# Kernel tuning notes

Hardware: AMD Instinct MI355X
Metric: run time of the kernel (lower is better)

Reference implementation:

```python
import jax, jax.numpy as jnp
import numpy as np

B = 1024
U = 2048

def setup_inputs() -> dict:
    key = jax.random.key(0)
    k1, k2, k3, k4 = jax.random.split(key, 4)
    x = jax.random.normal(k1, (B, U), dtype=jnp.float32)
    h = jax.random.normal(k2, (B, U), dtype=jnp.float32)
    c = jax.random.normal(k3, (B, U), dtype=jnp.float32)
    # keras 'uniform' initializer ~ U(-0.05, 0.05); scale similarly
    w = jax.random.uniform(k4, (2 * U, 4 * U), dtype=jnp.float32, minval=-0.05, maxval=0.05)
    return {"x": x, "h": h, "c": c, "w": w}

def reference(x, h, c, w):
    # concat -> matmul -> split into 4 gates -> gating
    xh = jnp.concatenate([x, h], axis=1)            # [B, 2U]
    ifgo = xh @ w                                   # [B, 4U]
    i, f, g, o = jnp.split(ifgo, 4, axis=1)
    i = jax.nn.sigmoid(i)
    f = jax.nn.sigmoid(f)
    o = jax.nn.sigmoid(o)
    g = jnp.tanh(g)
    c_new = f * c + i * g
    h_new = o * jnp.tanh(c_new)
    return (h_new, h_new, c_new)
```

## Files before the change

kernel.cpp:

```cpp
#include <hip/hip_runtime.h>


#define BDIM   1024
#define UDIM   2048
#define KDIM   4096
#define NDIM   8192

#define BM 128
#define BN 128
#define BK 64
#define NT (KDIM / BK)

typedef __attribute__((ext_vector_type(4))) float        f32x4;
typedef __attribute__((ext_vector_type(8))) short        short8;
typedef __attribute__((ext_vector_type(4))) unsigned int u32x4;

__device__ inline unsigned int cvt_pk_bf16(float lo, float hi) {
    unsigned int r;
    asm("v_cvt_pk_bf16_f32 %0, %1, %2" : "=v"(r) : "v"(lo), "v"(hi));
    return r;
}

__global__ __launch_bounds__(256, 2)
void lstm_gemm(const float* __restrict__ x, const float* __restrict__ h,
               const float* __restrict__ w, float* __restrict__ ifgo) {
    __shared__ unsigned short As[2][BM * BK];
    __shared__ unsigned short Bs[2][BN * BK];

    const int tid  = threadIdx.x;
    const int lane = tid & 63;
    const int wid  = tid >> 6;
    const int wr   = wid >> 1;
    const int wc   = wid & 1;
    const int lrow = lane & 15;
    const int lk   = lane >> 4;

    const int m0 = blockIdx.y * BM;
    const int n0 = blockIdx.x * BN;

    f32x4 acc[4][4];
#pragma unroll
    for (int i = 0; i < 4; ++i)
#pragma unroll
        for (int j = 0; j < 4; ++j)
            acc[i][j] = (f32x4){0.f, 0.f, 0.f, 0.f};

    f32x4 av[4][2];
    float bv[4][8];

    auto loadA = [&](int t) {
        int k0 = t * BK;
        const float* src = (k0 < UDIM) ? x + (size_t)m0 * UDIM + k0
                                       : h + (size_t)m0 * UDIM + (k0 - UDIM);
#pragma unroll
        for (int p = 0; p < 4; ++p) {
            int e = p * 256 + tid, arow = e >> 3, k8 = (e & 7) * 8;
            const float* gp = src + (size_t)arow * UDIM + k8;
            av[p][0] = *(const f32x4*)gp;
            av[p][1] = *(const f32x4*)(gp + 4);
        }
    };
    auto loadB = [&](int t) {
        int k0 = t * BK;
#pragma unroll
        for (int p = 0; p < 4; ++p) {
            int q = p * 256 + tid, n = q & 127, kg = q >> 7;
            const float* gp = w + (size_t)(k0 + kg * 8) * NDIM + n0 + n;
#pragma unroll
            for (int j = 0; j < 8; ++j) bv[p][j] = gp[(size_t)j * NDIM];
        }
    };
    auto writeAB = [&](int buf) {
        char* AsB = (char*)As[buf];
        char* BsB = (char*)Bs[buf];
#pragma unroll
        for (int p = 0; p < 4; ++p) {
            int e = p * 256 + tid, arow = e >> 3, k8 = (e & 7) * 8;
            u32x4 u;
            u[0] = cvt_pk_bf16(av[p][0][0], av[p][0][1]);
            u[1] = cvt_pk_bf16(av[p][0][2], av[p][0][3]);
            u[2] = cvt_pk_bf16(av[p][1][0], av[p][1][1]);
            u[3] = cvt_pk_bf16(av[p][1][2], av[p][1][3]);
            *(u32x4*)(AsB + arow * 128 + ((k8 * 2) ^ ((arow & 7) << 4))) = u;
        }
#pragma unroll
        for (int p = 0; p < 4; ++p) {
            int q = p * 256 + tid, n = q & 127, kg = q >> 7;
            u32x4 u;
#pragma unroll
            for (int j = 0; j < 4; ++j)
                u[j] = cvt_pk_bf16(bv[p][2 * j], bv[p][2 * j + 1]);
            *(u32x4*)(BsB + n * 128 + ((kg * 16) ^ ((n & 7) << 4))) = u;
        }
    };
    auto compute = [&](int buf) {
        const char* AsB = (const char*)As[buf];
        const char* BsB = (const char*)Bs[buf];
#pragma unroll
        for (int kk = 0; kk < 2; ++kk) {
            short8 af[4], bfr[4];
#pragma unroll
            for (int mi = 0; mi < 4; ++mi) {
                int row = wr * 64 + mi * 16 + lrow;
                int kb  = kk * 64 + lk * 16;
                af[mi] = *(const short8*)(AsB + row * 128 + (kb ^ ((row & 7) << 4)));
            }
#pragma unroll
            for (int ni = 0; ni < 4; ++ni) {
                int row = wc * 64 + ni * 16 + lrow;
                int kb  = kk * 64 + lk * 16;
                bfr[ni] = *(const short8*)(BsB + row * 128 + (kb ^ ((row & 7) << 4)));
            }
#pragma unroll
            for (int mi = 0; mi < 4; ++mi)
#pragma unroll
                for (int ni = 0; ni < 4; ++ni)
                    acc[mi][ni] = __builtin_amdgcn_mfma_f32_16x16x32_bf16(
                        af[mi], bfr[ni], acc[mi][ni], 0, 0, 0);
        }
    };

    loadA(0); loadB(0);
    writeAB(0);
    loadA(1); loadB(1);
    __syncthreads();

    for (int t = 0; t < NT; ++t) {
        int cur = t & 1;
        if (t + 1 < NT) {
            writeAB(cur ^ 1);
            if (t + 2 < NT) { loadA(t + 2); loadB(t + 2); }
        }
        compute(cur);
        __syncthreads();
    }

#pragma unroll
    for (int mi = 0; mi < 4; ++mi) {
        int grow = m0 + wr * 64 + mi * 16 + lk * 4;
#pragma unroll
        for (int ni = 0; ni < 4; ++ni) {
            int gcol = n0 + wc * 64 + ni * 16 + lrow;
            float* op = ifgo + (size_t)grow * NDIM + gcol;
#pragma unroll
            for (int r = 0; r < 4; ++r)
                op[(size_t)r * NDIM] = acc[mi][ni][r];
        }
    }
}

__device__ inline float fast_sigmoid(float v) {
    return __builtin_amdgcn_rcpf(1.f + __expf(-v));
}
__device__ inline float fast_tanh(float v) {
    float t = __expf(-2.f * __builtin_fabsf(v));
    float r = (1.f - t) * __builtin_amdgcn_rcpf(1.f + t);
    return __builtin_copysignf(r, v);
}

__global__ __launch_bounds__(256)
void lstm_gates(const float* __restrict__ ifgo, const float* __restrict__ c,
                float* __restrict__ out) {
    const int total4 = (BDIM * UDIM) / 4;
    int idx = blockIdx.x * blockDim.x + threadIdx.x;
    if (idx >= total4) return;
    int m  = idx >> 9;
    int u4 = idx & 511;
    const f32x4* base = (const f32x4*)(ifgo + (size_t)m * NDIM);
    f32x4 iv = base[u4];
    f32x4 fv = base[512 + u4];
    f32x4 gv = base[1024 + u4];
    f32x4 ov = base[1536 + u4];
    f32x4 cv = ((const f32x4*)c)[idx];
    f32x4 hn, cn;
#pragma unroll
    for (int r = 0; r < 4; ++r) {
        float ii = fast_sigmoid(iv[r]);
        float ff = fast_sigmoid(fv[r]);
        float oo = fast_sigmoid(ov[r]);
        float gg = fast_tanh(gv[r]);
        float cc = ff * cv[r] + ii * gg;
        cn[r] = cc;
        hn[r] = oo * fast_tanh(cc);
    }
    ((f32x4*)out)[idx] = hn;
    ((f32x4*)(out + (size_t)BDIM * UDIM))[idx] = hn;
    ((f32x4*)(out + (size_t)2 * BDIM * UDIM))[idx] = cn;
}

extern "C" void kernel_launch(void* const* d_in, const int* in_sizes, int n_in,
                              void* d_out, int out_size, void* d_ws, size_t ws_size,
                              hipStream_t stream) {
    const float* x = (const float*)d_in[0];
    const float* h = (const float*)d_in[1];
    const float* c = (const float*)d_in[2];
    const float* w = (const float*)d_in[3];
    float* ifgo = (float*)d_ws;
    float* out  = (float*)d_out;

    dim3 ggrid(NDIM / BN, BDIM / BM);
    lstm_gemm<<<ggrid, 256, 0, stream>>>(x, h, w, ifgo);

    int total4 = (BDIM * UDIM) / 4;
    lstm_gates<<<(total4 + 255) / 256, 256, 0, stream>>>(ifgo, c, out);
}
```

Measured before the change: 294.4 us.

## Fuse LSTM gate activations into GEMM epilogue by gathering all four gates per tile

Each GEMM tile now takes 32 units from each of the four gate column ranges, so one block holds i, f, g and o for the same units and applies the LSTM gating in its epilogue. This removes the 32 MB ifgo intermediate write and read and the second kernel launch. The warp layout changes from 2x2 to 4x1 (each warp covers 32 rows by 128 columns), which means more B fragment LDS reads per MFMA. The epilogue stores are now scalar and strided rather than vectorised.

```diff
diff --git a/kernel.cpp b/kernel.cpp
--- a/kernel.cpp
+++ b/kernel.cpp
@@ -5,9 +5,7 @@
 #define UDIM   2048
 #define KDIM   4096
 #define NDIM   8192
-
 #define BM 128
-#define BN 128
 #define BK 64
 #define NT (KDIM / BK)
 
@@ -20,29 +18,36 @@
     asm("v_cvt_pk_bf16_f32 %0, %1, %2" : "=v"(r) : "v"(lo), "v"(hi));
     return r;
 }
+__device__ inline float fast_sigmoid(float v) {
+    return __builtin_amdgcn_rcpf(1.f + __expf(-v));
+}
+__device__ inline float fast_tanh(float v) {
+    float t = __expf(-2.f * __builtin_fabsf(v));
+    float r = (1.f - t) * __builtin_amdgcn_rcpf(1.f + t);
+    return __builtin_copysignf(r, v);
+}
 
 __global__ __launch_bounds__(256, 2)
-void lstm_gemm(const float* __restrict__ x, const float* __restrict__ h,
-               const float* __restrict__ w, float* __restrict__ ifgo) {
+void lstm_fused(const float* __restrict__ x, const float* __restrict__ h,
+                const float* __restrict__ c, const float* __restrict__ w,
+                float* __restrict__ out) {
     __shared__ unsigned short As[2][BM * BK];
-    __shared__ unsigned short Bs[2][BN * BK];
+    __shared__ unsigned short Bs[2][BM * BK];
 
     const int tid  = threadIdx.x;
     const int lane = tid & 63;
     const int wid  = tid >> 6;
-    const int wr   = wid >> 1;
-    const int wc   = wid & 1;
     const int lrow = lane & 15;
     const int lk   = lane >> 4;
 
     const int m0 = blockIdx.y * BM;
-    const int n0 = blockIdx.x * BN;
+    const int u0 = blockIdx.x * 32;
 
-    f32x4 acc[4][4];
+    f32x4 acc[2][8];
 #pragma unroll
-    for (int i = 0; i < 4; ++i)
+    for (int i = 0; i < 2; ++i)
 #pragma unroll
-        for (int j = 0; j < 4; ++j)
+        for (int j = 0; j < 8; ++j)
             acc[i][j] = (f32x4){0.f, 0.f, 0.f, 0.f};
 
     f32x4 av[4][2];
@@ -64,8 +69,9 @@
         int k0 = t * BK;
 #pragma unroll
         for (int p = 0; p < 4; ++p) {
-            int q = p * 256 + tid, n = q & 127, kg = q >> 7;
-            const float* gp = w + (size_t)(k0 + kg * 8) * NDIM + n0 + n;
+            int q = p * 256 + tid, np = q & 127, kg = q >> 7;
+            int col = (np >> 5) * UDIM + u0 + (np & 31);
+            const float* gp = w + (size_t)(k0 + kg * 8) * NDIM + col;
 #pragma unroll
             for (int j = 0; j < 8; ++j) bv[p][j] = gp[(size_t)j * NDIM];
         }
@@ -85,12 +91,12 @@
         }
 #pragma unroll
         for (int p = 0; p < 4; ++p) {
-            int q = p * 256 + tid, n = q & 127, kg = q >> 7;
+            int q = p * 256 + tid, np = q & 127, kg = q >> 7;
             u32x4 u;
 #pragma unroll
             for (int j = 0; j < 4; ++j)
                 u[j] = cvt_pk_bf16(bv[p][2 * j], bv[p][2 * j + 1]);
-            *(u32x4*)(BsB + n * 128 + ((kg * 16) ^ ((n & 7) << 4))) = u;
+            *(u32x4*)(BsB + np * 128 + ((kg * 16) ^ ((np & 7) << 4))) = u;
         }
     };
     auto compute = [&](int buf) {
@@ -98,23 +104,22 @@
         const char* BsB = (const char*)Bs[buf];
 #pragma unroll
         for (int kk = 0; kk < 2; ++kk) {
-            short8 af[4], bfr[4];
+            short8 af[2], bfr[8];
+            int kb = kk * 64 + lk * 16;
 #pragma unroll
-            for (int mi = 0; mi < 4; ++mi) {
-                int row = wr * 64 + mi * 16 + lrow;
-                int kb  = kk * 64 + lk * 16;
+            for (int mi = 0; mi < 2; ++mi) {
+                int row = wid * 32 + mi * 16 + lrow;
                 af[mi] = *(const short8*)(AsB + row * 128 + (kb ^ ((row & 7) << 4)));
             }
 #pragma unroll
-            for (int ni = 0; ni < 4; ++ni) {
-                int row = wc * 64 + ni * 16 + lrow;
-                int kb  = kk * 64 + lk * 16;
+            for (int ni = 0; ni < 8; ++ni) {
+                int row = ni * 16 + lrow;
                 bfr[ni] = *(const short8*)(BsB + row * 128 + (kb ^ ((row & 7) << 4)));
             }
 #pragma unroll
-            for (int mi = 0; mi < 4; ++mi)
+            for (int mi = 0; mi < 2; ++mi)
 #pragma unroll
-                for (int ni = 0; ni < 4; ++ni)
+                for (int ni = 0; ni < 8; ++ni)
                     acc[mi][ni] = __builtin_amdgcn_mfma_f32_16x16x32_bf16(
                         af[mi], bfr[ni], acc[mi][ni], 0, 0, 0);
         }
@@ -135,57 +140,29 @@
         __syncthreads();
     }
 
+    const size_t M = (size_t)BDIM * UDIM;
 #pragma unroll
-    for (int mi = 0; mi < 4; ++mi) {
-        int grow = m0 + wr * 64 + mi * 16 + lk * 4;
+    for (int mi = 0; mi < 2; ++mi) {
+        int rbase = m0 + wid * 32 + mi * 16 + lk * 4;
 #pragma unroll
-        for (int ni = 0; ni < 4; ++ni) {
-            int gcol = n0 + wc * 64 + ni * 16 + lrow;
-            float* op = ifgo + (size_t)grow * NDIM + gcol;
+        for (int half = 0; half < 2; ++half) {
+            int u = u0 + half * 16 + lrow;
+            f32x4 iv = acc[mi][0 + half];
+            f32x4 fv = acc[mi][2 + half];
+            f32x4 gv = acc[mi][4 + half];
+            f32x4 ov = acc[mi][6 + half];
 #pragma unroll
-            for (int r = 0; r < 4; ++r)
-                op[(size_t)r * NDIM] = acc[mi][ni][r];
+            for (int r = 0; r < 4; ++r) {
+                size_t off = (size_t)(rbase + r) * UDIM + u;
+                float cc = fast_sigmoid(fv[r]) * c[off] +
+                           fast_sigmoid(iv[r]) * fast_tanh(gv[r]);
+                float hh = fast_sigmoid(ov[r]) * fast_tanh(cc);
+                out[off]         = hh;
+                out[M + off]     = hh;
+                out[2 * M + off] = cc;
+            }
         }
     }
-}
-
-__device__ inline float fast_sigmoid(float v) {
-    return __builtin_amdgcn_rcpf(1.f + __expf(-v));
-}
-__device__ inline float fast_tanh(float v) {
-    float t = __expf(-2.f * __builtin_fabsf(v));
-    float r = (1.f - t) * __builtin_amdgcn_rcpf(1.f + t);
-    return __builtin_copysignf(r, v);
-}
-
-__global__ __launch_bounds__(256)
-void lstm_gates(const float* __restrict__ ifgo, const float* __restrict__ c,
-                float* __restrict__ out) {
-    const int total4 = (BDIM * UDIM) / 4;
-    int idx = blockIdx.x * blockDim.x + threadIdx.x;
-    if (idx >= total4) return;
-    int m  = idx >> 9;
-    int u4 = idx & 511;
-    const f32x4* base = (const f32x4*)(ifgo + (size_t)m * NDIM);
-    f32x4 iv = base[u4];
-    f32x4 fv = base[512 + u4];
-    f32x4 gv = base[1024 + u4];
-    f32x4 ov = base[1536 + u4];
-    f32x4 cv = ((const f32x4*)c)[idx];
-    f32x4 hn, cn;
-#pragma unroll
-    for (int r = 0; r < 4; ++r) {
-        float ii = fast_sigmoid(iv[r]);
-        float ff = fast_sigmoid(fv[r]);
-        float oo = fast_sigmoid(ov[r]);
-        float gg = fast_tanh(gv[r]);
-        float cc = ff * cv[r] + ii * gg;
-        cn[r] = cc;
-        hn[r] = oo * fast_tanh(cc);
-    }
-    ((f32x4*)out)[idx] = hn;
-    ((f32x4*)(out + (size_t)BDIM * UDIM))[idx] = hn;
-    ((f32x4*)(out + (size_t)2 * BDIM * UDIM))[idx] = cn;
 }
 
 extern "C" void kernel_launch(void* const* d_in, const int* in_sizes, int n_in,
@@ -195,12 +172,8 @@
     const float* h = (const float*)d_in[1];
     const float* c = (const float*)d_in[2];
     const float* w = (const float*)d_in[3];
-    float* ifgo = (float*)d_ws;
-    float* out  = (float*)d_out;
+    float* out = (float*)d_out;
 
-    dim3 ggrid(NDIM / BN, BDIM / BM);
-    lstm_gemm<<<ggrid, 256, 0, stream>>>(x, h, w, ifgo);
-
-    int total4 = (BDIM * UDIM) / 4;
-    lstm_gates<<<(total4 + 255) / 256, 256, 0, stream>>>(ifgo, c, out);
+    dim3 grid(UDIM / 32, BDIM / BM);
+    lstm_fused<<<grid, 256, 0, stream>>>(x, h, c, w, out);
 }
```

Measured after the change: 300.7 us. +2.1%, slower.
